# Optimization experiments

Hardware: AMD Instinct MI355X
Metric: run time of the kernel (lower is better)

The kernel has to match this reference:

```python
import jax, jax.numpy as jnp
import numpy as np

B, T, D, H, L, C = 64, 256, 256, 512, 2, 1000

def setup_inputs() -> dict:
    key = jax.random.key(0)
    ks = jax.random.split(key, 11)
    s = 0.05
    return {
        "inp":   jax.random.normal(ks[0], (B, T, D), dtype=jnp.float32),
        "W_ih0": jax.random.normal(ks[1], (H, D), dtype=jnp.float32) * s,
        "W_hh0": jax.random.normal(ks[2], (H, H), dtype=jnp.float32) * s,
        "b_ih0": jax.random.normal(ks[3], (H,), dtype=jnp.float32) * s,
        "b_hh0": jax.random.normal(ks[4], (H,), dtype=jnp.float32) * s,
        "W_ih1": jax.random.normal(ks[5], (H, H), dtype=jnp.float32) * s,
        "W_hh1": jax.random.normal(ks[6], (H, H), dtype=jnp.float32) * s,
        "b_ih1": jax.random.normal(ks[7], (H,), dtype=jnp.float32) * s,
        "b_hh1": jax.random.normal(ks[8], (H,), dtype=jnp.float32) * s,
        "fc_w":  jax.random.normal(ks[9], (C, H * T), dtype=jnp.float32) * 0.01,
        "fc_b":  jax.random.normal(ks[10], (C,), dtype=jnp.float32) * s,
    }

def _rnn_layer(x, W_ih, W_hh, b_ih, b_hh):
    # x: [B, T, Din] -> out: [B, T, H]; h_t = tanh(x_t W_ih^T + b_ih + h_{t-1} W_hh^T + b_hh)
    xw = jnp.einsum('btd,hd->bth', x, W_ih) + (b_ih + b_hh)  # precompute input affine
    h0 = jnp.zeros((x.shape[0], W_hh.shape[0]), x.dtype)
    def step(h, xw_t):
        h_new = jnp.tanh(xw_t + h @ W_hh.T)
        return h_new, h_new
    _, ys = jax.lax.scan(step, h0, jnp.swapaxes(xw, 0, 1))  # [T, B, H]
    return jnp.swapaxes(ys, 0, 1)

def reference(inp, W_ih0, W_hh0, b_ih0, b_hh0, W_ih1, W_hh1, b_ih1, b_hh1, fc_w, fc_b):
    h = _rnn_layer(inp, W_ih0, W_hh0, b_ih0, b_hh0)
    h = _rnn_layer(h, W_ih1, W_hh1, b_ih1, b_hh1)
    flat = h.reshape(h.shape[0], -1)          # [B, T*H]
    return flat @ fc_w.T + fc_b               # [B, C]
```

## Files before the change

### kernel.cpp

```cpp
#include <hip/hip_runtime.h>
#include <hip/hip_bf16.h>
#include <hip/hip_fp16.h>

#define B_ 64
#define T_ 256
#define D_ 256
#define H_ 512
#define C_ 1000
#define M_ (B_*T_)
#define KFC (T_*H_)

typedef _Float16 f16x2 __attribute__((ext_vector_type(2)));
typedef _Float16 f16x4 __attribute__((ext_vector_type(4)));
typedef _Float16 f16x8 __attribute__((ext_vector_type(8)));
typedef float    f32x4 __attribute__((ext_vector_type(4)));

#if defined(__has_builtin)
#if __has_builtin(__builtin_amdgcn_fdot2)
#define FDOT2(w,h,acc) (acc) = __builtin_amdgcn_fdot2((w),(h),(acc),false)
#endif
#endif
#ifndef FDOT2
#define FDOT2(w,h,acc) (acc) += (float)(w)[0]*(float)(h)[0] + (float)(w)[1]*(float)(h)[1]
#endif

#define DOT8(wv,hv,d0,d1,d2,d3) do{                                            \
  f16x2 wa = __builtin_shufflevector((wv),(wv),0,1), ha = __builtin_shufflevector((hv),(hv),0,1); \
  f16x2 wb = __builtin_shufflevector((wv),(wv),2,3), hb = __builtin_shufflevector((hv),(hv),2,3); \
  f16x2 wc = __builtin_shufflevector((wv),(wv),4,5), hc = __builtin_shufflevector((hv),(hv),4,5); \
  f16x2 wd = __builtin_shufflevector((wv),(wv),6,7), hd = __builtin_shufflevector((hv),(hv),6,7); \
  FDOT2(wa,ha,d0); FDOT2(wb,hb,d1); FDOT2(wc,hc,d2); FDOT2(wd,hd,d3);          \
}while(0)

__device__ __forceinline__ float tanh_fast(float x){
  float e = __expf(2.0f*x);
  return 1.0f - 2.0f/(e + 1.0f);
}


__global__ void k_cvt_x(const float* __restrict__ x, _Float16* __restrict__ o){
  int i = (blockIdx.x*256 + threadIdx.x)*4;
  float4 v = *(const float4*)(x + i);
  f16x4 r = {(_Float16)v.x,(_Float16)v.y,(_Float16)v.z,(_Float16)v.w};
  *(f16x4*)(o + i) = r;
}

__global__ void k_pack_wb(const float* __restrict__ W, _Float16* __restrict__ WB, int K){
  int id = blockIdx.x*256 + threadIdx.x;
  int g  = id & 3;
  int n  = (id >> 2) & 511;
  int kt = id >> 11;
  const float* src = W + (size_t)n*K + kt*32 + g*8;
  _Float16* dst = WB + ((size_t)(kt*512 + n)*4 + g)*8;
  #pragma unroll
  for (int j=0;j<8;++j) dst[j] = (_Float16)src[j];
}

__global__ void k_pack_w8(const float* __restrict__ W, _Float16* __restrict__ W8){
  int id = blockIdx.x*256 + threadIdx.x;
  int n  = id & 511;
  int kc = id >> 9;
  const float* src = W + (size_t)n*512 + kc*8;
  _Float16* dst = W8 + (size_t)(kc*512 + n)*8;
  #pragma unroll
  for (int j=0;j<8;++j) dst[j] = (_Float16)src[j];
}

__global__ void k_bias(const float* __restrict__ a, const float* __restrict__ b,
                       float* __restrict__ o){
  int i = blockIdx.x*256 + threadIdx.x;
  if (i < 512) o[i] = a[i] + b[i];
}

template<int K>
__global__ __launch_bounds__(256,4) void k_affine(const _Float16* __restrict__ X,
        const _Float16* __restrict__ WB, float* __restrict__ XW){
  __shared__ __align__(16) char Asb[64*128];
  const int m0 = blockIdx.x*64, n0 = blockIdx.y*64;
  const int tid = threadIdx.x, lane = tid & 63, w = tid >> 6;
  f32x4 acc[4] = {{0,0,0,0},{0,0,0,0},{0,0,0,0},{0,0,0,0}};

  for (int kc = 0; kc < K; kc += 64){
    #pragma unroll
    for (int c = tid; c < 512; c += 256){
      int row = c >> 3, seg = c & 7;
      f16x8 v = *(const f16x8*)(X + (size_t)(m0+row)*K + kc + seg*8);
      *(f16x8*)(Asb + row*128 + (((seg ^ (row&7)))<<4)) = v;
    }
    __syncthreads();
    #pragma unroll
    for (int kt2 = 0; kt2 < 2; ++kt2){
      int kt = (kc >> 5) + kt2;
      f16x8 bf = *(const f16x8*)(WB + ((size_t)(kt*512 + n0 + w*16 + (lane&15))*4 + (lane>>4))*8);
      #pragma unroll
      for (int mt = 0; mt < 4; ++mt){
        int r  = mt*16 + (lane & 15);
        int x8 = kt2*4 + (lane >> 4);
        f16x8 af = *(const f16x8*)(Asb + r*128 + (((x8 ^ (r&7)))<<4));
        acc[mt] = __builtin_amdgcn_mfma_f32_16x16x32_f16(af, bf, acc[mt], 0,0,0);
      }
    }
    __syncthreads();
  }
  #pragma unroll
  for (int mt = 0; mt < 4; ++mt)
    #pragma unroll
    for (int j = 0; j < 4; ++j){
      int m = m0 + mt*16 + (lane>>4)*4 + j;
      int n = n0 + w*16 + (lane&15);
      XW[(size_t)m*512 + n] = acc[mt][j];
    }
}

#define KV2 45
#define KL2 (64-KV2)

template<int MODE>
__global__ __launch_bounds__(512,1) void k_rec2(const float* __restrict__ XW,
        const _Float16* __restrict__ W8, const float* __restrict__ bias,
        _Float16* __restrict__ OUT){
  extern __shared__ __align__(16) char smem[];
  _Float16* WL = (_Float16*)smem;
  _Float16* h2 = (_Float16*)(smem + (size_t)KL2*512*16);
  const int b = blockIdx.x, n = threadIdx.x;
  const float bia = bias[n];
  const f16x8* wp = ((const f16x8*)W8) + n;

  f16x8 wr[KV2];
  #pragma unroll
  for (int kc = 0; kc < KV2; ++kc) wr[kc] = wp[kc*512];
  f16x8* wl = ((f16x8*)WL) + n;
  #pragma unroll
  for (int j = 0; j < KL2; ++j) wl[j*512] = wp[(KV2+j)*512];
  h2[n] = (_Float16)0.0f;
  __syncthreads();

  const float* xp = XW + (size_t)(b<<8)*512 + n;
  float xv = xp[0];
  int cur = 0;
  for (int t = 0; t < 256; ++t){
    float xv_next = xp[(size_t)(t < 255 ? t+1 : t)*512];
    const f16x8* hp = (const f16x8*)(h2 + cur*512);
    float d0=0.f, d1=0.f, d2=0.f, d3=0.f;
    #pragma unroll
    for (int kc = 0; kc < KV2; ++kc){
      f16x8 hv = hp[kc];
      DOT8(wr[kc], hv, d0,d1,d2,d3);
    }
    #pragma unroll
    for (int j = 0; j < KL2; ++j){
      f16x8 hv = hp[KV2+j];
      f16x8 wv = wl[j*512];
      DOT8(wv, hv, d0,d1,d2,d3);
    }
    float y = tanh_fast(bia + xv + ((d0+d1)+(d2+d3)));
    if (MODE == 0) OUT[((size_t)(b<<8)+t)*512 + n] = (_Float16)y;
    else           OUT[(size_t)((t<<4) + (n>>5))*2048 + (b<<5) + (n&31)] = (_Float16)y;
    h2[(cur^1)*512 + n] = (_Float16)y;
    __syncthreads();
    cur ^= 1;
    xv = xv_next;
  }
}

__global__ __launch_bounds__(512,1) void k_fc(const float* __restrict__ W,
        const _Float16* __restrict__ FB, float* __restrict__ part){
  const int n0 = blockIdx.x*64;
  const int kb = blockIdx.y;
  const int k0 = kb*2048;
  const int tid = threadIdx.x, lane = tid & 63, w = tid >> 6;
  const int q = w >> 2, s = w & 3;
  f32x4 acc[2] = {{0,0,0,0},{0,0,0,0}};
  for (int ks = 0; ks < 2048; ks += 32){
    int kt = (k0 + ks) >> 5;
    f16x8 bf = *(const f16x8*)(FB + ((size_t)(kt*64 + s*16 + (lane&15))*4 + (lane>>4))*8);
    #pragma unroll
    for (int mt = 0; mt < 2; ++mt){
      int row = n0 + (q*2 + mt)*16 + (lane & 15);
      if (row > 999) row = 999;
      const float* ap = W + (size_t)row*KFC + k0 + ks + (lane>>4)*8;
      float4 a0 = *(const float4*)ap;
      float4 a1 = *(const float4*)(ap + 4);
      f16x8 af = {(_Float16)a0.x,(_Float16)a0.y,(_Float16)a0.z,(_Float16)a0.w,
                  (_Float16)a1.x,(_Float16)a1.y,(_Float16)a1.z,(_Float16)a1.w};
      acc[mt] = __builtin_amdgcn_mfma_f32_16x16x32_f16(af, bf, acc[mt], 0,0,0);
    }
  }
  #pragma unroll
  for (int mt = 0; mt < 2; ++mt)
    #pragma unroll
    for (int j = 0; j < 4; ++j){
      int n = n0 + (q*2 + mt)*16 + (lane>>4)*4 + j;
      int m = s*16 + (lane & 15);
      if (n < 1000) part[(size_t)kb*64000 + m*1000 + n] = acc[mt][j];
    }
}

__global__ void k_reduce(const float* __restrict__ part, const float* __restrict__ fcb,
                         float* __restrict__ out){
  int i = blockIdx.x*256 + threadIdx.x;
  if (i >= 64000) return;
  float sacc = fcb[i % 1000];
  #pragma unroll 8
  for (int kb = 0; kb < 64; ++kb) sacc += part[(size_t)kb*64000 + i];
  out[i] = sacc;
}

extern "C" void kernel_launch(void* const* d_in, const int* in_sizes, int n_in,
                              void* d_out, int out_size, void* d_ws, size_t ws_size,
                              hipStream_t stream) {
  const float* inp  = (const float*)d_in[0];
  const float* Wih0 = (const float*)d_in[1];
  const float* Whh0 = (const float*)d_in[2];
  const float* bih0 = (const float*)d_in[3];
  const float* bhh0 = (const float*)d_in[4];
  const float* Wih1 = (const float*)d_in[5];
  const float* Whh1 = (const float*)d_in[6];
  const float* bih1 = (const float*)d_in[7];
  const float* bhh1 = (const float*)d_in[8];
  const float* fcw  = (const float*)d_in[9];
  const float* fcb  = (const float*)d_in[10];
  float* out = (float*)d_out;
  char* ws = (char*)d_ws;

  _Float16* xf    = (_Float16*)(ws + 0);
  _Float16* WB0   = (_Float16*)(ws + 8388608);
  _Float16* WB1   = (_Float16*)(ws + 8650752);
  _Float16* W80   = (_Float16*)(ws + 9175040);
  _Float16* W81   = (_Float16*)(ws + 9699328);
  float*    bias0 = (float*)   (ws + 10223616);
  float*    bias1 = (float*)   (ws + 10225664);
  float*    xw    = (float*)   (ws + 10227712);
  _Float16* h0    = (_Float16*)(ws + 43782144);
  _Float16* flatB = (_Float16*)(ws + 60559360);
  float*    part  = (float*)   (ws + 77336576);

  const size_t lds_rec = (size_t)KL2*512*16 + 2*512*2;
  (void)hipFuncSetAttribute(reinterpret_cast<const void*>(k_rec2<0>),
                            hipFuncAttributeMaxDynamicSharedMemorySize, (int)lds_rec);
  (void)hipFuncSetAttribute(reinterpret_cast<const void*>(k_rec2<1>),
                            hipFuncAttributeMaxDynamicSharedMemorySize, (int)lds_rec);

  k_cvt_x  <<<4096,256,0,stream>>>(inp, xf);
  k_pack_wb<<<  64,256,0,stream>>>(Wih0, WB0, 256);
  k_pack_wb<<< 128,256,0,stream>>>(Wih1, WB1, 512);
  k_pack_w8<<< 128,256,0,stream>>>(Whh0, W80);
  k_pack_w8<<< 128,256,0,stream>>>(Whh1, W81);
  k_bias   <<<   2,256,0,stream>>>(bih0, bhh0, bias0);
  k_bias   <<<   2,256,0,stream>>>(bih1, bhh1, bias1);

  k_affine<256><<<dim3(256,8),256,0,stream>>>(xf, WB0, xw);
  k_rec2<0>    <<<64,512,lds_rec,stream>>>(xw, W80, bias0, h0);
  k_affine<512><<<dim3(256,8),256,0,stream>>>(h0, WB1, xw);
  k_rec2<1>    <<<64,512,lds_rec,stream>>>(xw, W81, bias1, flatB);
  k_fc   <<<dim3(16,64),512,0,stream>>>(fcw, flatB, part);
  k_reduce<<<250,256,0,stream>>>(part, fcb, out);
}
```

Baseline: 1.122 ms.

## Halve recurrent block to 256 threads, two hidden units per thread

The recurrent kernel now runs 256 threads per block, and each thread computes two output hidden units. Each h vector loaded from LDS is reused for two dot products, and more of W_hh stays in registers (2x48 f16x8 chunks per thread instead of 45), with the remainder kept in LDS. Opaque asm barriers pin the register-resident weights. The aim is to cut LDS traffic for h broadcasts and barrier cost per step. The risk is very high VGPR pressure, which may spill, and fewer waves to hide latency.

```diff
diff --git a/kernel.cpp b/kernel.cpp
--- a/kernel.cpp
+++ b/kernel.cpp
@@ -112,54 +112,80 @@
     }
 }
 
-#define KV2 45
-#define KL2 (64-KV2)
+#define KV 48
+#define KL (64-KV)
 
 template<int MODE>
-__global__ __launch_bounds__(512,1) void k_rec2(const float* __restrict__ XW,
+__global__ __launch_bounds__(256,1) void k_rec3(const float* __restrict__ XW,
         const _Float16* __restrict__ W8, const float* __restrict__ bias,
         _Float16* __restrict__ OUT){
   extern __shared__ __align__(16) char smem[];
   _Float16* WL = (_Float16*)smem;
-  _Float16* h2 = (_Float16*)(smem + (size_t)KL2*512*16);
+  _Float16* h2 = (_Float16*)(smem + (size_t)KL*512*16);
   const int b = blockIdx.x, n = threadIdx.x;
-  const float bia = bias[n];
-  const f16x8* wp = ((const f16x8*)W8) + n;
-
-  f16x8 wr[KV2];
-  #pragma unroll
-  for (int kc = 0; kc < KV2; ++kc) wr[kc] = wp[kc*512];
-  f16x8* wl = ((f16x8*)WL) + n;
-  #pragma unroll
-  for (int j = 0; j < KL2; ++j) wl[j*512] = wp[(KV2+j)*512];
+  const float biaA = bias[n], biaB = bias[n+256];
+  const f16x8* wp = (const f16x8*)W8;
+
+  {
+    f16x8* dst = (f16x8*)WL;
+    const f16x8* src = wp + (size_t)KV*512;
+    #pragma unroll 4
+    for (int u = n; u < KL*512; u += 256) dst[u] = src[u];
+  }
+  f16x8 wA[KV], wB[KV];
+  #pragma unroll
+  for (int kc = 0; kc < KV; ++kc){
+    wA[kc] = wp[(size_t)kc*512 + n];
+    wB[kc] = wp[(size_t)kc*512 + n + 256];
+  }
+  #pragma unroll
+  for (int kc = 0; kc < KV; ++kc){
+    asm volatile("" : "+v"(wA[kc]));
+    asm volatile("" : "+v"(wB[kc]));
+  }
   h2[n] = (_Float16)0.0f;
+  h2[n+256] = (_Float16)0.0f;
   __syncthreads();
 
-  const float* xp = XW + (size_t)(b<<8)*512 + n;
-  float xv = xp[0];
+  const float* xpA = XW + (size_t)(b<<8)*512 + n;
+  const float* xpB = xpA + 256;
+  float xvA = xpA[0], xvB = xpB[0];
   int cur = 0;
   for (int t = 0; t < 256; ++t){
-    float xv_next = xp[(size_t)(t < 255 ? t+1 : t)*512];
+    int tn = (t < 255) ? t+1 : t;
+    float xvA_n = xpA[(size_t)tn*512];
+    float xvB_n = xpB[(size_t)tn*512];
     const f16x8* hp = (const f16x8*)(h2 + cur*512);
-    float d0=0.f, d1=0.f, d2=0.f, d3=0.f;
-    #pragma unroll
-    for (int kc = 0; kc < KV2; ++kc){
+    const f16x8* wl = (const f16x8*)WL;
+    float a0=0.f,a1=0.f,a2=0.f,a3=0.f, c0=0.f,c1=0.f,c2=0.f,c3=0.f;
+    #pragma unroll
+    for (int kc = 0; kc < KV; ++kc){
       f16x8 hv = hp[kc];
-      DOT8(wr[kc], hv, d0,d1,d2,d3);
-    }
-    #pragma unroll
-    for (int j = 0; j < KL2; ++j){
-      f16x8 hv = hp[KV2+j];
-      f16x8 wv = wl[j*512];
-      DOT8(wv, hv, d0,d1,d2,d3);
-    }
-    float y = tanh_fast(bia + xv + ((d0+d1)+(d2+d3)));
-    if (MODE == 0) OUT[((size_t)(b<<8)+t)*512 + n] = (_Float16)y;
-    else           OUT[(size_t)((t<<4) + (n>>5))*2048 + (b<<5) + (n&31)] = (_Float16)y;
-    h2[(cur^1)*512 + n] = (_Float16)y;
+      DOT8(wA[kc], hv, a0,a1,a2,a3);
+      DOT8(wB[kc], hv, c0,c1,c2,c3);
+    }
+    #pragma unroll
+    for (int j = 0; j < KL; ++j){
+      f16x8 hv  = hp[KV+j];
+      f16x8 wvA = wl[j*512 + n];
+      f16x8 wvB = wl[j*512 + n + 256];
+      DOT8(wvA, hv, a0,a1,a2,a3);
+      DOT8(wvB, hv, c0,c1,c2,c3);
+    }
+    float yA = tanh_fast(biaA + xvA + ((a0+a1)+(a2+a3)));
+    float yB = tanh_fast(biaB + xvB + ((c0+c1)+(c2+c3)));
+    if (MODE == 0){
+      OUT[((size_t)(b<<8)+t)*512 + n]       = (_Float16)yA;
+      OUT[((size_t)(b<<8)+t)*512 + n + 256] = (_Float16)yB;
+    } else {
+      OUT[(size_t)((t<<4) + (n>>5))*2048 + (b<<5) + (n&31)]       = (_Float16)yA;
+      OUT[(size_t)((t<<4) + ((n+256)>>5))*2048 + (b<<5) + (n&31)] = (_Float16)yB;
+    }
+    h2[(cur^1)*512 + n]       = (_Float16)yA;
+    h2[(cur^1)*512 + n + 256] = (_Float16)yB;
     __syncthreads();
     cur ^= 1;
-    xv = xv_next;
+    xvA = xvA_n; xvB = xvB_n;
   }
 }
 
@@ -235,10 +261,10 @@
   _Float16* flatB = (_Float16*)(ws + 60559360);
   float*    part  = (float*)   (ws + 77336576);
 
-  const size_t lds_rec = (size_t)KL2*512*16 + 2*512*2;
-  (void)hipFuncSetAttribute(reinterpret_cast<const void*>(k_rec2<0>),
+  const size_t lds_rec = (size_t)KL*512*16 + 2*512*2;
+  (void)hipFuncSetAttribute(reinterpret_cast<const void*>(k_rec3<0>),
                             hipFuncAttributeMaxDynamicSharedMemorySize, (int)lds_rec);
-  (void)hipFuncSetAttribute(reinterpret_cast<const void*>(k_rec2<1>),
+  (void)hipFuncSetAttribute(reinterpret_cast<const void*>(k_rec3<1>),
                             hipFuncAttributeMaxDynamicSharedMemorySize, (int)lds_rec);
 
   k_cvt_x  <<<4096,256,0,stream>>>(inp, xf);
@@ -250,9 +276,9 @@
   k_bias   <<<   2,256,0,stream>>>(bih1, bhh1, bias1);
 
   k_affine<256><<<dim3(256,8),256,0,stream>>>(xf, WB0, xw);
-  k_rec2<0>    <<<64,512,lds_rec,stream>>>(xw, W80, bias0, h0);
+  k_rec3<0>    <<<64,256,lds_rec,stream>>>(xw, W80, bias0, h0);
   k_affine<512><<<dim3(256,8),256,0,stream>>>(h0, WB1, xw);
-  k_rec2<1>    <<<64,512,lds_rec,stream>>>(xw, W81, bias1, flatB);
+  k_rec3<1>    <<<64,256,lds_rec,stream>>>(xw, W81, bias1, flatB);
   k_fc   <<<dim3(16,64),512,0,stream>>>(fcw, flatB, part);
   k_reduce<<<250,256,0,stream>>>(part, fcb, out);
 }
```

Result: slower. 2.274 ms (+102.7%).

## Split recurrent dot product across thread pairs to keep all weights in registers

Applied to the files above, without the earlier changes.

The recurrent kernel now uses 1024 threads per batch row, with two threads per hidden unit, each handling half of the K dimension. Each thread holds 32 f16x8 weight chunks in registers, and the two partial sums are combined with a lane shuffle. This removes the shared-memory weight spill and the LDS traffic it caused on every timestep. In exchange, the block-wide barrier now spans twice as many threads, and per-thread register pressure stays high.

```diff
diff --git a/kernel.cpp b/kernel.cpp
--- a/kernel.cpp
+++ b/kernel.cpp
@@ -112,54 +112,48 @@
     }
 }
 
-#define KV2 45
-#define KL2 (64-KV2)
-
 template<int MODE>
-__global__ __launch_bounds__(512,1) void k_rec2(const float* __restrict__ XW,
+__global__ __launch_bounds__(1024,1) void k_rec5(const float* __restrict__ XW,
         const _Float16* __restrict__ W8, const float* __restrict__ bias,
         _Float16* __restrict__ OUT){
-  extern __shared__ __align__(16) char smem[];
-  _Float16* WL = (_Float16*)smem;
-  _Float16* h2 = (_Float16*)(smem + (size_t)KL2*512*16);
-  const int b = blockIdx.x, n = threadIdx.x;
-  const float bia = bias[n];
-  const f16x8* wp = ((const f16x8*)W8) + n;
-
-  f16x8 wr[KV2];
-  #pragma unroll
-  for (int kc = 0; kc < KV2; ++kc) wr[kc] = wp[kc*512];
-  f16x8* wl = ((f16x8*)WL) + n;
-  #pragma unroll
-  for (int j = 0; j < KL2; ++j) wl[j*512] = wp[(KV2+j)*512];
-  h2[n] = (_Float16)0.0f;
+  __shared__ __align__(16) _Float16 h2[2][512];
+  const int b = blockIdx.x, t0 = threadIdx.x;
+  const int r = t0 >> 1, half = t0 & 1;
+  const float bia = bias[r];
+  const f16x8* wp = (const f16x8*)W8;
+
+  f16x8 wr[32];
+  #pragma unroll
+  for (int kc = 0; kc < 32; ++kc)
+    wr[kc] = wp[(size_t)((half<<5)+kc)*512 + r];
+
+  if (t0 < 512) h2[0][t0] = (_Float16)0.0f;
   __syncthreads();
 
-  const float* xp = XW + (size_t)(b<<8)*512 + n;
+  const float* xp = XW + (size_t)(b<<8)*512 + r;
   float xv = xp[0];
   int cur = 0;
   for (int t = 0; t < 256; ++t){
-    float xv_next = xp[(size_t)(t < 255 ? t+1 : t)*512];
-    const f16x8* hp = (const f16x8*)(h2 + cur*512);
-    float d0=0.f, d1=0.f, d2=0.f, d3=0.f;
-    #pragma unroll
-    for (int kc = 0; kc < KV2; ++kc){
+    int tn = (t < 255) ? t+1 : t;
+    float xv_n = xp[(size_t)tn*512];
+    const f16x8* hp = (const f16x8*)(h2[cur] + (half<<8));
+    float d0=0.f,d1=0.f,d2=0.f,d3=0.f;
+    #pragma unroll
+    for (int kc = 0; kc < 32; ++kc){
       f16x8 hv = hp[kc];
       DOT8(wr[kc], hv, d0,d1,d2,d3);
     }
-    #pragma unroll
-    for (int j = 0; j < KL2; ++j){
-      f16x8 hv = hp[KV2+j];
-      f16x8 wv = wl[j*512];
-      DOT8(wv, hv, d0,d1,d2,d3);
-    }
-    float y = tanh_fast(bia + xv + ((d0+d1)+(d2+d3)));
-    if (MODE == 0) OUT[((size_t)(b<<8)+t)*512 + n] = (_Float16)y;
-    else           OUT[(size_t)((t<<4) + (n>>5))*2048 + (b<<5) + (n&31)] = (_Float16)y;
-    h2[(cur^1)*512 + n] = (_Float16)y;
+    float d = (d0+d1)+(d2+d3);
+    d += __shfl_xor(d, 1, 64);
+    float y = tanh_fast(bia + xv + d);
+    if (half == 0){
+      if (MODE == 0) OUT[((size_t)(b<<8)+t)*512 + r] = (_Float16)y;
+      else           OUT[(size_t)((t<<4) + (r>>5))*2048 + (b<<5) + (r&31)] = (_Float16)y;
+      h2[cur^1][r] = (_Float16)y;
+    }
     __syncthreads();
     cur ^= 1;
-    xv = xv_next;
+    xv = xv_n;
   }
 }
 
@@ -235,12 +229,6 @@
   _Float16* flatB = (_Float16*)(ws + 60559360);
   float*    part  = (float*)   (ws + 77336576);
 
-  const size_t lds_rec = (size_t)KL2*512*16 + 2*512*2;
-  (void)hipFuncSetAttribute(reinterpret_cast<const void*>(k_rec2<0>),
-                            hipFuncAttributeMaxDynamicSharedMemorySize, (int)lds_rec);
-  (void)hipFuncSetAttribute(reinterpret_cast<const void*>(k_rec2<1>),
-                            hipFuncAttributeMaxDynamicSharedMemorySize, (int)lds_rec);
-
   k_cvt_x  <<<4096,256,0,stream>>>(inp, xf);
   k_pack_wb<<<  64,256,0,stream>>>(Wih0, WB0, 256);
   k_pack_wb<<< 128,256,0,stream>>>(Wih1, WB1, 512);
@@ -250,9 +238,9 @@
   k_bias   <<<   2,256,0,stream>>>(bih1, bhh1, bias1);
 
   k_affine<256><<<dim3(256,8),256,0,stream>>>(xf, WB0, xw);
-  k_rec2<0>    <<<64,512,lds_rec,stream>>>(xw, W80, bias0, h0);
+  k_rec5<0>    <<<64,1024,0,stream>>>(xw, W80, bias0, h0);
   k_affine<512><<<dim3(256,8),256,0,stream>>>(h0, WB1, xw);
-  k_rec2<1>    <<<64,512,lds_rec,stream>>>(xw, W81, bias1, flatB);
+  k_rec5<1>    <<<64,1024,0,stream>>>(xw, W81, bias1, flatB);
   k_fc   <<<dim3(16,64),512,0,stream>>>(fcw, flatB, part);
   k_reduce<<<250,256,0,stream>>>(part, fcb, out);
 }
```

Result: slower. 2.211 ms (+97.1%).
